# Performance work log

Measured on AMD Instinct MI355X. Metric: run time of the kernel, lower is better.

Reference implementation:

```python
import jax, jax.numpy as jnp
import numpy as np

N1, N2, E = 256, 128, 4096

def _conv(x, w, b):
    # NCHW conv, 3x3, padding=1 (SAME), then ReLU
    y = jax.lax.conv_general_dilated(x, w, (1, 1), 'SAME',
                                     dimension_numbers=('NCHW', 'OIHW', 'NCHW'))
    return jax.nn.relu(y + b[None, :, None, None])

def _pool(x):
    return jax.lax.reduce_window(x, -jnp.inf, jax.lax.max,
                                 (1, 1, 2, 2), (1, 1, 2, 2), 'VALID')

def _sage(x, src, dst, wl, bl, wr, n):
    # torch_geometric SAGEConv: out = lin_l(mean_j x_src) + lin_r(x), then L2 normalize
    agg = jax.ops.segment_sum(x[src], dst, num_segments=n)
    cnt = jax.ops.segment_sum(jnp.ones((src.shape[0],), x.dtype), dst, num_segments=n)
    agg = agg / jnp.maximum(cnt, 1.0)[:, None]
    out = agg @ wl.T + bl + x @ wr.T
    return out / jnp.maximum(jnp.linalg.norm(out, axis=-1, keepdims=True), 1e-12)

def _diff_pool(x, adj, s):
    # torch_geometric dense_diff_pool
    s = jax.nn.softmax(s, axis=-1)
    out = jnp.einsum('bnc,bnf->bcf', s, x)
    out_adj = jnp.einsum('bnc,bnm,bmd->bcd', s, adj, s)
    link = adj - jnp.einsum('bnc,bmc->bnm', s, s)
    link_loss = jnp.sqrt(jnp.sum(link * link)) / adj.size
    ent_loss = jnp.mean(jnp.sum(-s * jnp.log(s + 1e-15), axis=-1))
    return out, out_adj, link_loss, ent_loss

def setup_inputs() -> dict:
    key = jax.random.key(0)
    ks = jax.random.split(key, 16)
    rn = lambda k, shape, sc: jax.random.normal(k, shape, jnp.float32) * sc
    inp = {}
    inp['inputs'] = jax.random.normal(ks[0], (1, 5, 512, 512), jnp.float32)
    inp['edge_index'] = jax.random.randint(ks[1], (2, E), 0, N1)
    chans = [(5, 32), (32, 64), (64, 128), (128, 256), (256, 256)]
    for i, (ci, co) in enumerate(chans):
        inp[f'w{i+1}'] = rn(ks[2 + i], (co, ci, 3, 3), 1.0 / np.sqrt(ci * 9))
        inp[f'b{i+1}'] = jnp.zeros((co,), jnp.float32)
    sdims = [(256, 128), (256, 128), (128, 2)]
    for i, (ci, co) in enumerate(sdims):
        inp[f'sage{i+1}_wl'] = rn(ks[7 + 2 * i], (co, ci), 1.0 / np.sqrt(ci))
        inp[f'sage{i+1}_bl'] = jnp.zeros((co,), jnp.float32)
        inp[f'sage{i+1}_wr'] = rn(ks[8 + 2 * i], (co, ci), 1.0 / np.sqrt(ci))
    return inp

def reference(inputs, edge_index, w1, b1, w2, b2, w3, b3, w4, b4, w5, b5,
              sage1_wl, sage1_bl, sage1_wr, sage2_wl, sage2_bl, sage2_wr,
              sage3_wl, sage3_bl, sage3_wr):
    x = _pool(_conv(inputs, w1, b1))
    x = _pool(_conv(x, w2, b2))
    x = _pool(_conv(x, w3, b3))
    x = _pool(_conv(x, w4, b4))
    x = _pool(_conv(x, w5, b5))            # [1,256,16,16]
    org = x.reshape(N1, N1)                # [256 nodes, 256 feats]
    src, dst = edge_index[0], edge_index[1]
    x1 = _sage(org, src, dst, sage1_wl, sage1_bl, sage1_wr, N1)
    s1 = _sage(org, src, dst, sage2_wl, sage2_bl, sage2_wr, N1)
    # dense adjacency (scipy coo->dense sums duplicate edges)
    adj1 = jnp.zeros((N1, N1), jnp.float32).at[src, dst].add(1.0)
    xp, adjp, ll1, el1 = _diff_pool(x1[None], adj1[None], s1[None])
    xp = xp.reshape(N2, N2)
    adjp = adjp.reshape(N2, N2)
    # vectorized form of the per-row in-place argmax binarization loop
    row_max = jnp.max(adjp, axis=1, keepdims=True)
    edge_out = jnp.where(adjp == row_max, 1.0, 0.0)
    # dense_to_sparse of the binarized matrix (one max per row, generic case)
    cols = jnp.argmax(adjp, axis=1)
    ei2 = jnp.stack([jnp.arange(N2), cols])  # [2,128] int
    nodes_out = jnp.tanh(_sage(xp, ei2[0], ei2[1], sage3_wl, sage3_bl, sage3_wr, N2))
    adj2 = jnp.zeros((N2, N2), jnp.float32).at[ei2[0], ei2[1]].add(1.0)
    s2 = jnp.ones((1, N2, 1), jnp.float32)  # softmax over size-1 dim -> ones
    x2, _, ll2, el2 = _diff_pool(nodes_out[None], adj2[None], s2)
    return (x2.reshape(-1), ll1 + ll2, el1 + el2, nodes_out, edge_out, ei2)
```

## Files before the change

### kernel.cpp

```cpp
#include <hip/hip_runtime.h>
#include <hip/hip_bf16.h>
#include <math.h>

#define N_EDGES 4096
#define NN1 256
#define NN2 128

typedef short v8s __attribute__((ext_vector_type(8)));
typedef float v4f __attribute__((ext_vector_type(4)));

__device__ inline unsigned short f2b(float f){
  union { __hip_bfloat16 h; unsigned short u; } cv;
  cv.h = __float2bfloat16(f);
  return cv.u;
}

template<int NT>
__device__ inline float block_sum(float v, float* red, int t){
  red[t] = v; __syncthreads();
  #pragma unroll
  for (int st = NT/2; st > 0; st >>= 1){
    if (t < st) red[t] += red[t+st];
    __syncthreads();
  }
  float r = red[0]; __syncthreads();
  return r;
}
template<int NT>
__device__ inline float block_max(float v, float* red, int t){
  red[t] = v; __syncthreads();
  #pragma unroll
  for (int st = NT/2; st > 0; st >>= 1){
    if (t < st) red[t] = fmaxf(red[t], red[t+st]);
    __syncthreads();
  }
  float r = red[0]; __syncthreads();
  return r;
}
template<int NT>
__device__ inline int block_min_int(int v, int* red, int t){
  red[t] = v; __syncthreads();
  #pragma unroll
  for (int st = NT/2; st > 0; st >>= 1){
    if (t < st) red[t] = min(red[t], red[t+st]);
    __syncthreads();
  }
  int r = red[0]; __syncthreads();
  return r;
}

template<int CHUNKS, int COUT, int CIN, int SSLABS, int BSTR, int OUTF32>
__global__ __launch_bounds__(256) void conv_mfma(
    const unsigned short* __restrict__ in, const unsigned short* __restrict__ wb,
    const float* __restrict__ bias, unsigned short* __restrict__ outb,
    float* __restrict__ outf,
    int in_row, int in_slab, int out_row, int out_slab)
{
  constexpr int CG = COUT/32;
  __shared__ unsigned short tileb[SSLABS*2600];
  __shared__ unsigned short wldsb[9*32*40];

  const int cg = blockIdx.x % CG, bx = blockIdx.x / CG, by = blockIdx.y;
  const int tid = threadIdx.x, lane = tid & 63, wv = tid >> 6;
  const int cot = wv >> 1, wp = wv & 1;
  const int ml = lane & 15, g = lane >> 4;

  v4f acc[8];
  #pragma unroll
  for (int t = 0; t < 8; ++t) acc[t] = (v4f){0.f,0.f,0.f,0.f};

  for (int cb = 0; cb < CHUNKS; ++cb){
    if (cb) __syncthreads();
    for (int j = tid; j < SSLABS*324; j += 256){
      int s = j / 324, rem = j - s*324;
      int row = rem / 18, px = rem - row*18;
      int gidx = (cb*SSLABS + s)*in_slab + ((by*16 + row)*in_row + bx*16 + px)*8;
      *(v8s*)&tileb[s*2600 + (row*18+px)*8] = *(const v8s*)&in[gidx];
    }
    for (int j = tid; j < 1152; j += 256){
      int k = j >> 7, rem = j & 127;
      int co = rem >> 2, q = rem & 3;
      int gw = (k*COUT + cg*32 + co)*CIN + cb*32 + q*8;
      *(v8s*)&wldsb[(k*32+co)*40 + q*8] = *(const v8s*)&wb[gw];
    }
    __syncthreads();

    #pragma unroll
    for (int k9 = 0; k9 < 9; ++k9){
      const int ky = k9/3, kx = k9 - 3*(k9/3);
      v8s a = *(const v8s*)&wldsb[(k9*32 + cot*16 + ml)*40 + g*8];
      #pragma unroll
      for (int tt = 0; tt < 8; ++tt){
        int t = wp*8 + tt;
        v8s b = *(const v8s*)&tileb[g*BSTR + ((t+ky)*18 + kx + ml)*8];
        acc[tt] = __builtin_amdgcn_mfma_f32_16x16x32_bf16(a, b, acc[tt], 0, 0, 0);
      }
    }
  }

  const int cob = cg*32 + cot*16 + g*4;
  float b4[4] = {bias[cob], bias[cob+1], bias[cob+2], bias[cob+3]};
  #pragma unroll
  for (int tp = 0; tp < 4; ++tp){
    float m[4];
    #pragma unroll
    for (int r = 0; r < 4; ++r){
      float v = fmaxf(acc[2*tp][r], acc[2*tp+1][r]);
      float o = __shfl_xor(v, 1);
      m[r] = fmaxf(fmaxf(v, o) + b4[r], 0.f);
    }
    if ((lane & 1) == 0){
      int gy = by*8 + wp*4 + tp, gx = bx*8 + (ml >> 1);
      if (OUTF32){
        #pragma unroll
        for (int r = 0; r < 4; ++r)
          outf[(cob + r)*256 + gy*16 + gx] = m[r];
      } else {
        unsigned int u0 = (unsigned)f2b(m[0]) | ((unsigned)f2b(m[1]) << 16);
        unsigned int u1 = (unsigned)f2b(m[2]) | ((unsigned)f2b(m[3]) << 16);
        int slabo = cob >> 3, sub = (g & 1)*4;
        size_t idx = (size_t)slabo*out_slab + (size_t)((gy+1)*out_row + gx+1)*8 + sub;
        *(uint2*)(outb + idx) = make_uint2(u0, u1);
      }
    }
  }
}

__global__ __launch_bounds__(256) void zero_kernel(unsigned short* __restrict__ wsb,
                                                   float* __restrict__ adjz)
{
  int j = blockIdx.x*256 + threadIdx.x;
  const int c0=2056, c1=6184, c2=10344, c3=14568, c4=18920, ca=35368;
  if (j >= ca) return;
  if (j >= c4){
    int q = j - c4;
    ((float4*)adjz)[q] = make_float4(0.f,0.f,0.f,0.f);
    return;
  }
  int base, P, R, W, per, rem;
  if (j < c0)      { base=0;       P=516; R=514; W=512; per=2056; rem=j; }
  else if (j < c1) { base=2121792; P=260; R=258; W=256; per=1032; rem=j-c0; }
  else if (j < c2) { base=4268352; P=132; R=130; W=128; per=520;  rem=j-c1; }
  else if (j < c3) { base=5366592; P=68;  R=66;  W=64;  per=264;  rem=j-c2; }
  else             { base=5941056; P=36;  R=34;  W=32;  per=136;  rem=j-c3; }
  int s = rem / per, r2 = rem - s*per;
  int row, px;
  if (r2 < 2*P){ row = (r2 < P) ? 0 : R-1; px = (r2 < P) ? r2 : r2 - P; }
  else { int q = r2 - 2*P; row = 1 + (q >> 1); px = (q & 1) ? (W+1) : 0; }
  *(uint4*)&wsb[(size_t)base + ((size_t)(s*R + row)*P + px)*8] = make_uint4(0,0,0,0);
}

__global__ __launch_bounds__(256) void prep_kernel(
    const float* __restrict__ src, unsigned short* __restrict__ p0b,
    const float* __restrict__ w1, const float* __restrict__ w2,
    const float* __restrict__ w3, const float* __restrict__ w4,
    const float* __restrict__ w5, unsigned short* __restrict__ wbb,
    const float* __restrict__ a, const float* __restrict__ b2,
    const float* __restrict__ c2, const float* __restrict__ d2,
    float* __restrict__ o)
{
  int b = blockIdx.x, tid = threadIdx.x;
  if (b < 1024){
    int idx = b*256 + tid;
    int y = idx >> 9, x = idx & 511;
    unsigned short v8[8];
    #pragma unroll
    for (int c = 0; c < 5; ++c) v8[c] = f2b(src[c*262144 + y*512 + x]);
    v8[5] = 0; v8[6] = 0; v8[7] = 0;
    *(uint4*)&p0b[((size_t)(y+1)*516 + (x+1))*8] = *(uint4*)v8;
  } else if (b < 1452){
    int j = (b-1024)*256 + tid;
    int co, ci, CO, CIl, CIsrc, dst; const float* w;
    if (j < 1024)      { co=j>>5;        ci=j&31;        w=w1; CIsrc=5;   CO=32;  CIl=32;  dst=0; }
    else if (j < 3072) { int q=j-1024;   co=q>>5;  ci=q&31;  w=w2; CIsrc=32;  CO=64;  CIl=32;  dst=9216; }
    else if (j < 11264){ int q=j-3072;   co=q>>6;  ci=q&63;  w=w3; CIsrc=64;  CO=128; CIl=64;  dst=27648; }
    else if (j < 44032){ int q=j-11264;  co=q>>7;  ci=q&127; w=w4; CIsrc=128; CO=256; CIl=128; dst=101376; }
    else               { int q=j-44032;  co=q>>8;  ci=q&255; w=w5; CIsrc=256; CO=256; CIl=256; dst=396288; }
    #pragma unroll
    for (int k = 0; k < 9; ++k){
      float val = (ci < CIsrc) ? w[(co*CIsrc + ci)*9 + k] : 0.f;
      wbb[dst + (k*CO + co)*CIl + ci] = f2b(val);
    }
  } else {
    int idx = (b-1452)*256 + tid;
    int m = idx >> 15, rem = idx & 32767, k = rem >> 7, cc = rem & 127;
    const float* sp = (m==0)?a:(m==1)?b2:(m==2)?c2:d2;
    o[m*32768 + k*128 + cc] = sp[cc*256 + k];
  }
}

__global__ void build_adj_kernel(const int* __restrict__ ei, float* adj, float* cnt){
  int e = blockIdx.x*256 + threadIdx.x;
  if (e < N_EDGES){
    int s = ei[e], d = ei[N_EDGES + e];
    atomicAdd(&adj[s*NN1 + d], 1.0f);
    atomicAdd(&cnt[d], 1.0f);
  }
}

__global__ __launch_bounds__(128) void sage12_kernel(
    const float* __restrict__ adj, const float* __restrict__ cnt,
    const float* __restrict__ org,
    const float* __restrict__ wl1t, const float* __restrict__ bl1, const float* __restrict__ wr1t,
    const float* __restrict__ wl2t, const float* __restrict__ bl2, const float* __restrict__ wr2t,
    float* __restrict__ x1, float* __restrict__ s_out, float* __restrict__ st,
    float* __restrict__ entpart)
{
  __shared__ float sa[NN1], so[NN1], col[NN1], red[128];
  int n = blockIdx.x, c = threadIdx.x;
  for (int k = c; k < NN1; k += 128){
    col[k] = adj[k*NN1 + n];
    so[k]  = org[n*NN1 + k];
  }
  __syncthreads();
  float a0 = 0.f, a1 = 0.f;
  #pragma unroll 4
  for (int s2 = 0; s2 < NN1; ++s2){
    float av = col[s2];
    a0 += av * org[s2*NN1 + c];
    a1 += av * org[s2*NN1 + c + 128];
  }
  float cd = fmaxf(cnt[n], 1.0f);
  sa[c] = a0 / cd;
  sa[c+128] = a1 / cd;
  __syncthreads();

  float p1 = bl1[c], p2 = bl2[c];
  for (int k = 0; k < NN1; ++k){
    float av = sa[k], ov = so[k];
    p1 += av*wl1t[k*128+c] + ov*wr1t[k*128+c];
    p2 += av*wl2t[k*128+c] + ov*wr2t[k*128+c];
  }
  float n1s = block_sum<128>(p1*p1, red, c);
  x1[n*128 + c] = p1 / fmaxf(sqrtf(n1s), 1e-12f);
  float n2s = block_sum<128>(p2*p2, red, c);
  float p2n = p2 / fmaxf(sqrtf(n2s), 1e-12f);
  float mx = block_max<128>(p2n, red, c);
  float ev = expf(p2n - mx);
  float ssum = block_sum<128>(ev, red, c);
  float sv = ev / ssum;
  s_out[n*128 + c] = sv;
  st[c*NN1 + n] = sv;
  float esum = block_sum<128>(-sv * logf(sv + 1e-15f), red, c);
  if (c == 0) entpart[n] = esum;
}

__global__ __launch_bounds__(256) void fuse1_kernel(
    const float* __restrict__ s, const float* __restrict__ x1,
    const float* __restrict__ adj, const float* __restrict__ st,
    float* __restrict__ xp, float* __restrict__ t, float* __restrict__ linkpart)
{
  __shared__ float sn[128]; __shared__ float red[256];
  int b = blockIdx.x, tid = threadIdx.x;
  if (b < 64){
    int cc = b*2 + (tid >> 7), f = tid & 127;
    float acc = 0.f;
    for (int n = 0; n < NN1; ++n) acc += s[n*128+cc] * x1[n*128+f];
    xp[cc*128+f] = acc;
  } else if (b < 192){
    int n = (b-64)*2 + (tid >> 7), c = tid & 127;
    float acc = 0.f;
    for (int m = 0; m < NN1; ++m){
      float a = adj[n*NN1+m];
      if (a != 0.f) acc += a * s[m*128+c];
    }
    t[n*128+c] = acc;
  } else {
    int n = b - 192, m = tid;
    if (m < 128) sn[m] = s[n*128+m];
    __syncthreads();
    float dot = 0.f;
    for (int c = 0; c < 128; ++c) dot += sn[c]*st[c*NN1 + m];
    float v = adj[n*NN1+m] - dot;
    float part = block_sum<256>(v*v, red, m);
    if (m == 0) linkpart[n] = part;
  }
}

__global__ __launch_bounds__(128) void adjp_bin_kernel(
    const float* __restrict__ s, const float* __restrict__ t,
    float* __restrict__ edge_out, float* __restrict__ ei2_out, int* __restrict__ cols)
{
  __shared__ float scol[NN1]; __shared__ float red[128]; __shared__ int redi[128];
  int cc = blockIdx.x, j = threadIdx.x;
  scol[j]       = s[j*128 + cc];
  scol[j + 128] = s[(j+128)*128 + cc];
  __syncthreads();
  float acc = 0.f;
  for (int n = 0; n < NN1; ++n) acc += scol[n] * t[n*128 + j];
  float mx = block_max<128>(acc, red, j);
  edge_out[cc*128+j] = (acc == mx) ? 1.0f : 0.0f;
  int cand = (acc == mx) ? j : (1 << 30);
  int cmin = block_min_int<128>(cand, redi, j);
  if (j == 0){
    cols[cc] = cmin;
    ei2_out[cc] = (float)cc;
    ei2_out[128 + cc] = (float)cmin;
  }
}

__global__ __launch_bounds__(128) void sage3_kernel(
    const float* __restrict__ xp, const int* __restrict__ cols,
    const float* __restrict__ wl3, const float* __restrict__ bl3,
    const float* __restrict__ wr3, float* __restrict__ nodes_out)
{
  __shared__ int colsl[NN2]; __shared__ float red[128];
  int n = blockIdx.x, f = threadIdx.x;
  colsl[f] = cols[f];
  __syncthreads();
  float acc = 0.f, c = 0.f;
  for (int i = 0; i < NN2; ++i){
    if (colsl[i] == n){ acc += xp[i*128+f]; c += 1.f; }
  }
  float ag = acc / fmaxf(c, 1.f);
  float xv = xp[n*128+f];
  float q0 = block_sum<128>(ag*wl3[f]     + xv*wr3[f],     red, f);
  float q1 = block_sum<128>(ag*wl3[128+f] + xv*wr3[128+f], red, f);
  if (f == 0){
    float p0 = q0 + bl3[0], p1 = q1 + bl3[1];
    float nm = fmaxf(sqrtf(p0*p0 + p1*p1), 1e-12f);
    nodes_out[n*2+0] = tanhf(p0/nm);
    nodes_out[n*2+1] = tanhf(p1/nm);
  }
}

__global__ __launch_bounds__(256) void finalize_kernel(const float* __restrict__ linkpart,
    const float* __restrict__ entpart, float* __restrict__ d_out)
{
  __shared__ float red[256];
  int t = threadIdx.x;
  float ls = block_sum<256>(linkpart[t], red, t);
  float es = block_sum<256>(entpart[t], red, t);
  float v0 = 0.f, v1 = 0.f;
  if (t < 128){ v0 = d_out[4 + t*2 + 0]; v1 = d_out[4 + t*2 + 1]; }
  float s0 = block_sum<256>(v0, red, t);
  float s1 = block_sum<256>(v1, red, t);
  if (t == 0){
    d_out[0] = s0;
    d_out[1] = s1;
    d_out[2] = sqrtf(ls)/65536.0f + sqrtf(16256.0f)/16384.0f;
    d_out[3] = es/256.0f;
  }
}

extern "C" void kernel_launch(void* const* d_in, const int* in_sizes, int n_in,
                              void* d_out_v, int out_size, void* d_ws, size_t ws_size,
                              hipStream_t stream)
{
  (void)in_sizes; (void)n_in; (void)out_size; (void)ws_size;
  const float* input = (const float*)d_in[0];
  const int*   ei    = (const int*)  d_in[1];
  const float* w1 = (const float*)d_in[2];  const float* b1 = (const float*)d_in[3];
  const float* w2 = (const float*)d_in[4];  const float* b2 = (const float*)d_in[5];
  const float* w3 = (const float*)d_in[6];  const float* b3 = (const float*)d_in[7];
  const float* w4 = (const float*)d_in[8];  const float* b4 = (const float*)d_in[9];
  const float* w5 = (const float*)d_in[10]; const float* b5 = (const float*)d_in[11];
  const float* s1wl = (const float*)d_in[12]; const float* s1bl = (const float*)d_in[13];
  const float* s1wr = (const float*)d_in[14];
  const float* s2wl = (const float*)d_in[15]; const float* s2bl = (const float*)d_in[16];
  const float* s2wr = (const float*)d_in[17];
  const float* s3wl = (const float*)d_in[18]; const float* s3bl = (const float*)d_in[19];
  const float* s3wr = (const float*)d_in[20];
  float* d_out = (float*)d_out_v;
  float* ws = (float*)d_ws;

  unsigned short* P0b = (unsigned short*)(ws);
  unsigned short* Pb1 = (unsigned short*)(ws + 1060896);
  unsigned short* Pb2 = (unsigned short*)(ws + 2134176);
  unsigned short* Pb3 = (unsigned short*)(ws + 2683296);
  unsigned short* Pb4 = (unsigned short*)(ws + 2970528);
  unsigned short* wb  = (unsigned short*)(ws + 3127200);
  float* org = ws + 3620256;
  float* wt  = ws + 3685792;
  float* st  = ws + 3816864;
  float* G   = ws + 3849632;

  float* adj1     = G;
  float* cnt      = G + 65536;
  float* x1       = G + 147712;
  float* s        = G + 180480;
  float* t        = G + 213248;
  float* xp       = G + 246016;
  int*   cols     = (int*)(G + 278784);
  float* linkpart = G + 278912;
  float* entpart  = G + 279168;

  zero_kernel<<<dim3(139), 256, 0, stream>>>((unsigned short*)ws, adj1);
  prep_kernel<<<dim3(1964), 256, 0, stream>>>(input, P0b, w1, w2, w3, w4, w5, wb,
                                              s1wl, s1wr, s2wl, s2wr, wt);

  conv_mfma<1,32,32,1,0,0>      <<<dim3(32,32), 256, 0, stream>>>(P0b, wb,        b1, Pb1, nullptr, 516, 2121792, 260, 536640);
  conv_mfma<1,64,32,4,2600,0>   <<<dim3(32,16), 256, 0, stream>>>(Pb1, wb+9216,   b2, Pb2, nullptr, 260, 536640, 132, 137280);
  conv_mfma<2,128,64,4,2600,0>  <<<dim3(32,8),  256, 0, stream>>>(Pb2, wb+27648,  b3, Pb3, nullptr, 132, 137280, 68,  35904);
  conv_mfma<4,256,128,4,2600,0> <<<dim3(32,4),  256, 0, stream>>>(Pb3, wb+101376, b4, Pb4, nullptr, 68,  35904,  36,  9792);
  conv_mfma<8,256,256,4,2600,1> <<<dim3(16,2),  256, 0, stream>>>(Pb4, wb+396288, b5, nullptr, org, 36,  9792,   0,   0);

  build_adj_kernel<<<dim3(16),  256, 0, stream>>>(ei, adj1, cnt);
  sage12_kernel   <<<dim3(256), 128, 0, stream>>>(adj1, cnt, org, wt, s1bl, wt+32768,
                                                  wt+65536, s2bl, wt+98304, x1, s, st, entpart);
  fuse1_kernel    <<<dim3(448), 256, 0, stream>>>(s, x1, adj1, st, xp, t, linkpart);
  adjp_bin_kernel <<<dim3(128), 128, 0, stream>>>(s, t, d_out + 260, d_out + 16644, cols);
  sage3_kernel    <<<dim3(128), 128, 0, stream>>>(xp, cols, s3wl, s3bl, s3wr, d_out + 4);
  finalize_kernel <<<dim3(1),   256, 0, stream>>>(linkpart, entpart, d_out);
}
```

Measured before the change: 209.9 us.

## Double-buffer conv input tiles, load weights directly to registers, fold zeroing into prep

The conv kernel now double-buffers the input tile in shared memory, prefetching the next channel chunk into registers while the current chunk is computed, which removes one barrier per chunk. Weights are read straight from global memory into registers instead of being staged through a shared-memory tile. The separate zeroing kernel is merged into prep_kernel as extra blocks, saving one launch. In exchange, shared-memory use and register pressure go up, and the per-lane weight loads from global memory may be less coalesced.

```diff
diff --git a/kernel.cpp b/kernel.cpp
--- a/kernel.cpp
+++ b/kernel.cpp
@@ -56,45 +56,70 @@
     float* __restrict__ outf,
     int in_row, int in_slab, int out_row, int out_slab)
 {
-  constexpr int CG = COUT/32;
-  __shared__ unsigned short tileb[SSLABS*2600];
-  __shared__ unsigned short wldsb[9*32*40];
+  constexpr int CG  = COUT/32;
+  constexpr int TJ  = SSLABS*324;
+  constexpr int NST = (TJ + 255) / 256;
+  __shared__ unsigned short tileb[2][SSLABS*2600];
 
   const int cg = blockIdx.x % CG, bx = blockIdx.x / CG, by = blockIdx.y;
   const int tid = threadIdx.x, lane = tid & 63, wv = tid >> 6;
   const int cot = wv >> 1, wp = wv & 1;
   const int ml = lane & 15, g = lane >> 4;
 
-  v4f acc[8];
-  #pragma unroll
-  for (int t = 0; t < 8; ++t) acc[t] = (v4f){0.f,0.f,0.f,0.f};
-
-  for (int cb = 0; cb < CHUNKS; ++cb){
-    if (cb) __syncthreads();
-    for (int j = tid; j < SSLABS*324; j += 256){
+  int tsrc[NST], tlds[NST];
+  #pragma unroll
+  for (int s2 = 0; s2 < NST; ++s2){
+    int j = tid + s2*256;
+    if (j < TJ){
       int s = j / 324, rem = j - s*324;
       int row = rem / 18, px = rem - row*18;
-      int gidx = (cb*SSLABS + s)*in_slab + ((by*16 + row)*in_row + bx*16 + px)*8;
-      *(v8s*)&tileb[s*2600 + (row*18+px)*8] = *(const v8s*)&in[gidx];
-    }
-    for (int j = tid; j < 1152; j += 256){
-      int k = j >> 7, rem = j & 127;
-      int co = rem >> 2, q = rem & 3;
-      int gw = (k*COUT + cg*32 + co)*CIN + cb*32 + q*8;
-      *(v8s*)&wldsb[(k*32+co)*40 + q*8] = *(const v8s*)&wb[gw];
-    }
-    __syncthreads();
-
+      tsrc[s2] = s*in_slab + ((by*16 + row)*in_row + bx*16 + px)*8;
+      tlds[s2] = s*2600 + (row*18+px)*8;
+    } else { tsrc[s2] = -1; tlds[s2] = 0; }
+  }
+  const int wbase = (cg*32 + cot*16 + ml)*CIN + g*8;
+
+  v4f acc[8];
+  #pragma unroll
+  for (int t = 0; t < 8; ++t) acc[t] = (v4f){0.f,0.f,0.f,0.f};
+
+  uint4 rt[NST];
+  auto LD = [&](int cb){
+    int off = cb*SSLABS*in_slab;
+    #pragma unroll
+    for (int s2 = 0; s2 < NST; ++s2)
+      if (tsrc[s2] >= 0) rt[s2] = *(const uint4*)&in[tsrc[s2] + off];
+  };
+  auto ST = [&](int b){
+    #pragma unroll
+    for (int s2 = 0; s2 < NST; ++s2)
+      if (tsrc[s2] >= 0) *(uint4*)&tileb[b][tlds[s2]] = rt[s2];
+  };
+  auto COMPUTE = [&](int b, int cb){
+    v8s wa[9];
+    const int wo = wbase + cb*32;
+    #pragma unroll
+    for (int k = 0; k < 9; ++k)
+      wa[k] = *(const v8s*)&wb[k*COUT*CIN + wo];
     #pragma unroll
     for (int k9 = 0; k9 < 9; ++k9){
       const int ky = k9/3, kx = k9 - 3*(k9/3);
-      v8s a = *(const v8s*)&wldsb[(k9*32 + cot*16 + ml)*40 + g*8];
       #pragma unroll
       for (int tt = 0; tt < 8; ++tt){
         int t = wp*8 + tt;
-        v8s b = *(const v8s*)&tileb[g*BSTR + ((t+ky)*18 + kx + ml)*8];
-        acc[tt] = __builtin_amdgcn_mfma_f32_16x16x32_bf16(a, b, acc[tt], 0, 0, 0);
+        v8s bfr = *(const v8s*)&tileb[b][g*BSTR + ((t+ky)*18 + kx + ml)*8];
+        acc[tt] = __builtin_amdgcn_mfma_f32_16x16x32_bf16(wa[k9], bfr, acc[tt], 0, 0, 0);
       }
+    }
+  };
+
+  LD(0); ST(0); __syncthreads();
+  for (int cb = 0; cb < CHUNKS; ++cb){
+    if (cb + 1 < CHUNKS) LD(cb+1);
+    COMPUTE(cb & 1, cb);
+    if (cb + 1 < CHUNKS){
+      ST((cb+1) & 1);
+      __syncthreads();
     }
   }
 
@@ -126,30 +151,6 @@
   }
 }
 
-__global__ __launch_bounds__(256) void zero_kernel(unsigned short* __restrict__ wsb,
-                                                   float* __restrict__ adjz)
-{
-  int j = blockIdx.x*256 + threadIdx.x;
-  const int c0=2056, c1=6184, c2=10344, c3=14568, c4=18920, ca=35368;
-  if (j >= ca) return;
-  if (j >= c4){
-    int q = j - c4;
-    ((float4*)adjz)[q] = make_float4(0.f,0.f,0.f,0.f);
-    return;
-  }
-  int base, P, R, W, per, rem;
-  if (j < c0)      { base=0;       P=516; R=514; W=512; per=2056; rem=j; }
-  else if (j < c1) { base=2121792; P=260; R=258; W=256; per=1032; rem=j-c0; }
-  else if (j < c2) { base=4268352; P=132; R=130; W=128; per=520;  rem=j-c1; }
-  else if (j < c3) { base=5366592; P=68;  R=66;  W=64;  per=264;  rem=j-c2; }
-  else             { base=5941056; P=36;  R=34;  W=32;  per=136;  rem=j-c3; }
-  int s = rem / per, r2 = rem - s*per;
-  int row, px;
-  if (r2 < 2*P){ row = (r2 < P) ? 0 : R-1; px = (r2 < P) ? r2 : r2 - P; }
-  else { int q = r2 - 2*P; row = 1 + (q >> 1); px = (q & 1) ? (W+1) : 0; }
-  *(uint4*)&wsb[(size_t)base + ((size_t)(s*R + row)*P + px)*8] = make_uint4(0,0,0,0);
-}
-
 __global__ __launch_bounds__(256) void prep_kernel(
     const float* __restrict__ src, unsigned short* __restrict__ p0b,
     const float* __restrict__ w1, const float* __restrict__ w2,
@@ -157,7 +158,8 @@
     const float* __restrict__ w5, unsigned short* __restrict__ wbb,
     const float* __restrict__ a, const float* __restrict__ b2,
     const float* __restrict__ c2, const float* __restrict__ d2,
-    float* __restrict__ o)
+    float* __restrict__ o, unsigned short* __restrict__ wsb,
+    float* __restrict__ adjz)
 {
   int b = blockIdx.x, tid = threadIdx.x;
   if (b < 1024){
@@ -181,11 +183,31 @@
       float val = (ci < CIsrc) ? w[(co*CIsrc + ci)*9 + k] : 0.f;
       wbb[dst + (k*CO + co)*CIl + ci] = f2b(val);
     }
-  } else {
+  } else if (b < 1964){
     int idx = (b-1452)*256 + tid;
     int m = idx >> 15, rem = idx & 32767, k = rem >> 7, cc = rem & 127;
     const float* sp = (m==0)?a:(m==1)?b2:(m==2)?c2:d2;
     o[m*32768 + k*128 + cc] = sp[cc*256 + k];
+  } else {
+    int j = (b-1964)*256 + tid;
+    const int c0=2056, c1=6184, c2z=10344, c3=14568, c4=18920, ca=35368;
+    if (j >= ca) return;
+    if (j >= c4){
+      int q = j - c4;
+      ((float4*)adjz)[q] = make_float4(0.f,0.f,0.f,0.f);
+      return;
+    }
+    int base, P, R, W, per, rem;
+    if (j < c0)       { base=0;       P=516; R=514; W=512; per=2056; rem=j; }
+    else if (j < c1)  { base=2121792; P=260; R=258; W=256; per=1032; rem=j-c0; }
+    else if (j < c2z) { base=4268352; P=132; R=130; W=128; per=520;  rem=j-c1; }
+    else if (j < c3)  { base=5366592; P=68;  R=66;  W=64;  per=264;  rem=j-c2z; }
+    else              { base=5941056; P=36;  R=34;  W=32;  per=136;  rem=j-c3; }
+    int s = rem / per, r2 = rem - s*per;
+    int row, px;
+    if (r2 < 2*P){ row = (r2 < P) ? 0 : R-1; px = (r2 < P) ? r2 : r2 - P; }
+    else { int q = r2 - 2*P; row = 1 + (q >> 1); px = (q & 1) ? (W+1) : 0; }
+    *(uint4*)&wsb[(size_t)base + ((size_t)(s*R + row)*P + px)*8] = make_uint4(0,0,0,0);
   }
 }
 
@@ -385,9 +407,9 @@
   float* linkpart = G + 278912;
   float* entpart  = G + 279168;
 
-  zero_kernel<<<dim3(139), 256, 0, stream>>>((unsigned short*)ws, adj1);
-  prep_kernel<<<dim3(1964), 256, 0, stream>>>(input, P0b, w1, w2, w3, w4, w5, wb,
-                                              s1wl, s1wr, s2wl, s2wr, wt);
+  prep_kernel<<<dim3(2103), 256, 0, stream>>>(input, P0b, w1, w2, w3, w4, w5, wb,
+                                              s1wl, s1wr, s2wl, s2wr, wt,
+                                              (unsigned short*)ws, adj1);
 
   conv_mfma<1,32,32,1,0,0>      <<<dim3(32,32), 256, 0, stream>>>(P0b, wb,        b1, Pb1, nullptr, 516, 2121792, 260, 536640);
   conv_mfma<1,64,32,4,2600,0>   <<<dim3(32,16), 256, 0, stream>>>(Pb1, wb+9216,   b2, Pb2, nullptr, 260, 536640, 132, 137280);
```

Measured after the change: 219.8 us. 4.7% more time.

## Fuse graph tail kernels into one cooperative kernel and merge zeroing into prep

Applied to the files above, without the earlier changes.

Replaces the six small tail kernels (adjacency build, two SAGE layers, diff-pool fusion, argmax binarization, finalize) with one cooperative kernel of 256 blocks that uses grid-wide syncs between stages. It also folds the zero kernel into the prep kernel as extra blocks, so two fewer launches happen at the front. The aim is to remove launch and inter-kernel gap overhead in the latency-bound tail. In exchange there are five grid.sync barriers, and some stages leave half the threads idle because blocks are now 256 wide where the work was sized for 128.

```diff
diff --git a/kernel.cpp b/kernel.cpp
--- a/kernel.cpp
+++ b/kernel.cpp
@@ -1,6 +1,9 @@
 #include <hip/hip_runtime.h>
 #include <hip/hip_bf16.h>
+#include <hip/hip_cooperative_groups.h>
 #include <math.h>
+
+namespace cg = cooperative_groups;
 
 #define N_EDGES 4096
 #define NN1 256
@@ -15,33 +18,30 @@
   return cv.u;
 }
 
-template<int NT>
-__device__ inline float block_sum(float v, float* red, int t){
+__device__ inline float bsum(float v, float* red, int t){
   red[t] = v; __syncthreads();
   #pragma unroll
-  for (int st = NT/2; st > 0; st >>= 1){
+  for (int st = 128; st > 0; st >>= 1){
     if (t < st) red[t] += red[t+st];
     __syncthreads();
   }
   float r = red[0]; __syncthreads();
   return r;
 }
-template<int NT>
-__device__ inline float block_max(float v, float* red, int t){
+__device__ inline float bmax(float v, float* red, int t){
   red[t] = v; __syncthreads();
   #pragma unroll
-  for (int st = NT/2; st > 0; st >>= 1){
+  for (int st = 128; st > 0; st >>= 1){
     if (t < st) red[t] = fmaxf(red[t], red[t+st]);
     __syncthreads();
   }
   float r = red[0]; __syncthreads();
   return r;
 }
-template<int NT>
-__device__ inline int block_min_int(int v, int* red, int t){
+__device__ inline int bmin_i(int v, int* red, int t){
   red[t] = v; __syncthreads();
   #pragma unroll
-  for (int st = NT/2; st > 0; st >>= 1){
+  for (int st = 128; st > 0; st >>= 1){
     if (t < st) red[t] = min(red[t], red[t+st]);
     __syncthreads();
   }
@@ -126,30 +126,6 @@
   }
 }
 
-__global__ __launch_bounds__(256) void zero_kernel(unsigned short* __restrict__ wsb,
-                                                   float* __restrict__ adjz)
-{
-  int j = blockIdx.x*256 + threadIdx.x;
-  const int c0=2056, c1=6184, c2=10344, c3=14568, c4=18920, ca=35368;
-  if (j >= ca) return;
-  if (j >= c4){
-    int q = j - c4;
-    ((float4*)adjz)[q] = make_float4(0.f,0.f,0.f,0.f);
-    return;
-  }
-  int base, P, R, W, per, rem;
-  if (j < c0)      { base=0;       P=516; R=514; W=512; per=2056; rem=j; }
-  else if (j < c1) { base=2121792; P=260; R=258; W=256; per=1032; rem=j-c0; }
-  else if (j < c2) { base=4268352; P=132; R=130; W=128; per=520;  rem=j-c1; }
-  else if (j < c3) { base=5366592; P=68;  R=66;  W=64;  per=264;  rem=j-c2; }
-  else             { base=5941056; P=36;  R=34;  W=32;  per=136;  rem=j-c3; }
-  int s = rem / per, r2 = rem - s*per;
-  int row, px;
-  if (r2 < 2*P){ row = (r2 < P) ? 0 : R-1; px = (r2 < P) ? r2 : r2 - P; }
-  else { int q = r2 - 2*P; row = 1 + (q >> 1); px = (q & 1) ? (W+1) : 0; }
-  *(uint4*)&wsb[(size_t)base + ((size_t)(s*R + row)*P + px)*8] = make_uint4(0,0,0,0);
-}
-
 __global__ __launch_bounds__(256) void prep_kernel(
     const float* __restrict__ src, unsigned short* __restrict__ p0b,
     const float* __restrict__ w1, const float* __restrict__ w2,
@@ -157,7 +133,8 @@
     const float* __restrict__ w5, unsigned short* __restrict__ wbb,
     const float* __restrict__ a, const float* __restrict__ b2,
     const float* __restrict__ c2, const float* __restrict__ d2,
-    float* __restrict__ o)
+    float* __restrict__ o, unsigned short* __restrict__ wsb,
+    float* __restrict__ adjz)
 {
   int b = blockIdx.x, tid = threadIdx.x;
   if (b < 1024){
@@ -181,165 +158,183 @@
       float val = (ci < CIsrc) ? w[(co*CIsrc + ci)*9 + k] : 0.f;
       wbb[dst + (k*CO + co)*CIl + ci] = f2b(val);
     }
-  } else {
+  } else if (b < 1964){
     int idx = (b-1452)*256 + tid;
     int m = idx >> 15, rem = idx & 32767, k = rem >> 7, cc = rem & 127;
     const float* sp = (m==0)?a:(m==1)?b2:(m==2)?c2:d2;
     o[m*32768 + k*128 + cc] = sp[cc*256 + k];
-  }
-}
-
-__global__ void build_adj_kernel(const int* __restrict__ ei, float* adj, float* cnt){
-  int e = blockIdx.x*256 + threadIdx.x;
-  if (e < N_EDGES){
-    int s = ei[e], d = ei[N_EDGES + e];
-    atomicAdd(&adj[s*NN1 + d], 1.0f);
-    atomicAdd(&cnt[d], 1.0f);
-  }
-}
-
-__global__ __launch_bounds__(128) void sage12_kernel(
-    const float* __restrict__ adj, const float* __restrict__ cnt,
-    const float* __restrict__ org,
-    const float* __restrict__ wl1t, const float* __restrict__ bl1, const float* __restrict__ wr1t,
-    const float* __restrict__ wl2t, const float* __restrict__ bl2, const float* __restrict__ wr2t,
-    float* __restrict__ x1, float* __restrict__ s_out, float* __restrict__ st,
-    float* __restrict__ entpart)
+  } else {
+    int j = (b-1964)*256 + tid;
+    const int c0=2056, c1=6184, c2z=10344, c3=14568, c4=18920, ca=35368;
+    if (j >= ca) return;
+    if (j >= c4){
+      int q = j - c4;
+      ((float4*)adjz)[q] = make_float4(0.f,0.f,0.f,0.f);
+      return;
+    }
+    int base, P, R, W, per, rem;
+    if (j < c0)       { base=0;       P=516; R=514; W=512; per=2056; rem=j; }
+    else if (j < c1)  { base=2121792; P=260; R=258; W=256; per=1032; rem=j-c0; }
+    else if (j < c2z) { base=4268352; P=132; R=130; W=128; per=520;  rem=j-c1; }
+    else if (j < c3)  { base=5366592; P=68;  R=66;  W=64;  per=264;  rem=j-c2z; }
+    else              { base=5941056; P=36;  R=34;  W=32;  per=136;  rem=j-c3; }
+    int s = rem / per, r2 = rem - s*per;
+    int row, px;
+    if (r2 < 2*P){ row = (r2 < P) ? 0 : R-1; px = (r2 < P) ? r2 : r2 - P; }
+    else { int q = r2 - 2*P; row = 1 + (q >> 1); px = (q & 1) ? (W+1) : 0; }
+    *(uint4*)&wsb[(size_t)base + ((size_t)(s*R + row)*P + px)*8] = make_uint4(0,0,0,0);
+  }
+}
+
+__global__ __launch_bounds__(256) void coop_tail(
+    const int* ei, float* adj, float* cnt, const float* org, const float* wt,
+    const float* s1bl, const float* s2bl, float* x1, float* s, float* st,
+    float* entpart, float* xp, float* t, float* linkpart,
+    const float* s3wl, const float* s3bl, const float* s3wr,
+    float* d_out, int* cols)
 {
-  __shared__ float sa[NN1], so[NN1], col[NN1], red[128];
-  int n = blockIdx.x, c = threadIdx.x;
-  for (int k = c; k < NN1; k += 128){
-    col[k] = adj[k*NN1 + n];
-    so[k]  = org[n*NN1 + k];
-  }
-  __syncthreads();
-  float a0 = 0.f, a1 = 0.f;
-  #pragma unroll 4
-  for (int s2 = 0; s2 < NN1; ++s2){
-    float av = col[s2];
-    a0 += av * org[s2*NN1 + c];
-    a1 += av * org[s2*NN1 + c + 128];
-  }
-  float cd = fmaxf(cnt[n], 1.0f);
-  sa[c] = a0 / cd;
-  sa[c+128] = a1 / cd;
-  __syncthreads();
-
-  float p1 = bl1[c], p2 = bl2[c];
-  for (int k = 0; k < NN1; ++k){
-    float av = sa[k], ov = so[k];
-    p1 += av*wl1t[k*128+c] + ov*wr1t[k*128+c];
-    p2 += av*wl2t[k*128+c] + ov*wr2t[k*128+c];
-  }
-  float n1s = block_sum<128>(p1*p1, red, c);
-  x1[n*128 + c] = p1 / fmaxf(sqrtf(n1s), 1e-12f);
-  float n2s = block_sum<128>(p2*p2, red, c);
-  float p2n = p2 / fmaxf(sqrtf(n2s), 1e-12f);
-  float mx = block_max<128>(p2n, red, c);
-  float ev = expf(p2n - mx);
-  float ssum = block_sum<128>(ev, red, c);
-  float sv = ev / ssum;
-  s_out[n*128 + c] = sv;
-  st[c*NN1 + n] = sv;
-  float esum = block_sum<128>(-sv * logf(sv + 1e-15f), red, c);
-  if (c == 0) entpart[n] = esum;
-}
-
-__global__ __launch_bounds__(256) void fuse1_kernel(
-    const float* __restrict__ s, const float* __restrict__ x1,
-    const float* __restrict__ adj, const float* __restrict__ st,
-    float* __restrict__ xp, float* __restrict__ t, float* __restrict__ linkpart)
-{
-  __shared__ float sn[128]; __shared__ float red[256];
-  int b = blockIdx.x, tid = threadIdx.x;
-  if (b < 64){
-    int cc = b*2 + (tid >> 7), f = tid & 127;
+  cg::grid_group grid = cg::this_grid();
+  __shared__ float shA[256], shB[256], shC[256], shRed[256];
+  __shared__ int shRedI[256];
+  const int b = blockIdx.x, tid = threadIdx.x;
+
+  if (tid < 16){
+    int e = b*16 + tid;
+    int sn = ei[e], dn = ei[N_EDGES + e];
+    atomicAdd(&adj[sn*NN1 + dn], 1.0f);
+    atomicAdd(&cnt[dn], 1.0f);
+  }
+  grid.sync();
+
+  {
+    const int n = b;
+    const float* wl1t = wt;         const float* wr1t = wt + 32768;
+    const float* wl2t = wt + 65536; const float* wr2t = wt + 98304;
+    shC[tid] = adj[tid*NN1 + n];
+    shB[tid] = org[n*NN1 + tid];
+    __syncthreads();
+    float a0 = 0.f;
+    #pragma unroll 4
+    for (int s2 = 0; s2 < NN1; ++s2) a0 += shC[s2] * org[s2*NN1 + tid];
+    float cd = fmaxf(cnt[n], 1.0f);
+    shA[tid] = a0 / cd;
+    __syncthreads();
+
+    const int c = tid & 127;
+    float p1 = 0.f, p2 = 0.f;
+    if (tid < 128){
+      p1 = s1bl[c]; p2 = s2bl[c];
+      for (int k = 0; k < NN1; ++k){
+        float av = shA[k], ov = shB[k];
+        p1 += av*wl1t[k*128+c] + ov*wr1t[k*128+c];
+        p2 += av*wl2t[k*128+c] + ov*wr2t[k*128+c];
+      }
+    }
+    float n1s = bsum(tid < 128 ? p1*p1 : 0.f, shRed, tid);
+    if (tid < 128) x1[n*128 + c] = p1 / fmaxf(sqrtf(n1s), 1e-12f);
+    float n2s = bsum(tid < 128 ? p2*p2 : 0.f, shRed, tid);
+    float p2n = p2 / fmaxf(sqrtf(n2s), 1e-12f);
+    float mx = bmax(tid < 128 ? p2n : -INFINITY, shRed, tid);
+    float ev = expf(p2n - mx);
+    float ssum = bsum(tid < 128 ? ev : 0.f, shRed, tid);
+    float sv = ev / ssum;
+    if (tid < 128){
+      s[n*128 + c] = sv;
+      st[c*NN1 + n] = sv;
+    }
+    float esum = bsum(tid < 128 ? (-sv * logf(sv + 1e-15f)) : 0.f, shRed, tid);
+    if (tid == 0) entpart[n] = esum;
+  }
+  grid.sync();
+
+  {
+    if (b < 64){
+      int cc = b*2 + (tid >> 7), f = tid & 127;
+      float acc = 0.f;
+      for (int n2 = 0; n2 < NN1; ++n2) acc += s[n2*128+cc] * x1[n2*128+f];
+      xp[cc*128+f] = acc;
+    } else if (b < 192){
+      int n2 = (b-64)*2 + (tid >> 7), c = tid & 127;
+      float acc = 0.f;
+      for (int m = 0; m < NN1; ++m){
+        float a = adj[n2*NN1+m];
+        if (a != 0.f) acc += a * s[m*128+c];
+      }
+      t[n2*128+c] = acc;
+    }
+    __syncthreads();
+    if (tid < 128) shC[tid] = s[b*128 + tid];
+    __syncthreads();
+    float dot = 0.f;
+    for (int c2 = 0; c2 < 128; ++c2) dot += shC[c2]*st[c2*NN1 + tid];
+    float v = adj[b*NN1+tid] - dot;
+    float part = bsum(v*v, shRed, tid);
+    if (tid == 0) linkpart[b] = part;
+  }
+  grid.sync();
+
+  if (b < 128){
+    int cc = b;
+    shA[tid] = s[tid*128 + cc];
+    __syncthreads();
     float acc = 0.f;
-    for (int n = 0; n < NN1; ++n) acc += s[n*128+cc] * x1[n*128+f];
-    xp[cc*128+f] = acc;
-  } else if (b < 192){
-    int n = (b-64)*2 + (tid >> 7), c = tid & 127;
-    float acc = 0.f;
-    for (int m = 0; m < NN1; ++m){
-      float a = adj[n*NN1+m];
-      if (a != 0.f) acc += a * s[m*128+c];
-    }
-    t[n*128+c] = acc;
-  } else {
-    int n = b - 192, m = tid;
-    if (m < 128) sn[m] = s[n*128+m];
-    __syncthreads();
-    float dot = 0.f;
-    for (int c = 0; c < 128; ++c) dot += sn[c]*st[c*NN1 + m];
-    float v = adj[n*NN1+m] - dot;
-    float part = block_sum<256>(v*v, red, m);
-    if (m == 0) linkpart[n] = part;
-  }
-}
-
-__global__ __launch_bounds__(128) void adjp_bin_kernel(
-    const float* __restrict__ s, const float* __restrict__ t,
-    float* __restrict__ edge_out, float* __restrict__ ei2_out, int* __restrict__ cols)
-{
-  __shared__ float scol[NN1]; __shared__ float red[128]; __shared__ int redi[128];
-  int cc = blockIdx.x, j = threadIdx.x;
-  scol[j]       = s[j*128 + cc];
-  scol[j + 128] = s[(j+128)*128 + cc];
-  __syncthreads();
-  float acc = 0.f;
-  for (int n = 0; n < NN1; ++n) acc += scol[n] * t[n*128 + j];
-  float mx = block_max<128>(acc, red, j);
-  edge_out[cc*128+j] = (acc == mx) ? 1.0f : 0.0f;
-  int cand = (acc == mx) ? j : (1 << 30);
-  int cmin = block_min_int<128>(cand, redi, j);
-  if (j == 0){
-    cols[cc] = cmin;
-    ei2_out[cc] = (float)cc;
-    ei2_out[128 + cc] = (float)cmin;
-  }
-}
-
-__global__ __launch_bounds__(128) void sage3_kernel(
-    const float* __restrict__ xp, const int* __restrict__ cols,
-    const float* __restrict__ wl3, const float* __restrict__ bl3,
-    const float* __restrict__ wr3, float* __restrict__ nodes_out)
-{
-  __shared__ int colsl[NN2]; __shared__ float red[128];
-  int n = blockIdx.x, f = threadIdx.x;
-  colsl[f] = cols[f];
-  __syncthreads();
-  float acc = 0.f, c = 0.f;
-  for (int i = 0; i < NN2; ++i){
-    if (colsl[i] == n){ acc += xp[i*128+f]; c += 1.f; }
-  }
-  float ag = acc / fmaxf(c, 1.f);
-  float xv = xp[n*128+f];
-  float q0 = block_sum<128>(ag*wl3[f]     + xv*wr3[f],     red, f);
-  float q1 = block_sum<128>(ag*wl3[128+f] + xv*wr3[128+f], red, f);
-  if (f == 0){
-    float p0 = q0 + bl3[0], p1 = q1 + bl3[1];
-    float nm = fmaxf(sqrtf(p0*p0 + p1*p1), 1e-12f);
-    nodes_out[n*2+0] = tanhf(p0/nm);
-    nodes_out[n*2+1] = tanhf(p1/nm);
-  }
-}
-
-__global__ __launch_bounds__(256) void finalize_kernel(const float* __restrict__ linkpart,
-    const float* __restrict__ entpart, float* __restrict__ d_out)
-{
-  __shared__ float red[256];
-  int t = threadIdx.x;
-  float ls = block_sum<256>(linkpart[t], red, t);
-  float es = block_sum<256>(entpart[t], red, t);
-  float v0 = 0.f, v1 = 0.f;
-  if (t < 128){ v0 = d_out[4 + t*2 + 0]; v1 = d_out[4 + t*2 + 1]; }
-  float s0 = block_sum<256>(v0, red, t);
-  float s1 = block_sum<256>(v1, red, t);
-  if (t == 0){
-    d_out[0] = s0;
-    d_out[1] = s1;
-    d_out[2] = sqrtf(ls)/65536.0f + sqrtf(16256.0f)/16384.0f;
-    d_out[3] = es/256.0f;
+    int j = tid & 127;
+    if (tid < 128){
+      for (int n2 = 0; n2 < NN1; ++n2) acc += shA[n2] * t[n2*128 + j];
+    }
+    float mx = bmax(tid < 128 ? acc : -INFINITY, shRed, tid);
+    if (tid < 128) d_out[260 + cc*128 + j] = (acc == mx) ? 1.0f : 0.0f;
+    int cand = (tid < 128 && acc == mx) ? j : (1 << 30);
+    int cmin = bmin_i(cand, shRedI, tid);
+    if (tid == 0){
+      cols[cc] = cmin;
+      d_out[16644 + cc]       = (float)cc;
+      d_out[16644 + 128 + cc] = (float)cmin;
+    }
+  }
+  grid.sync();
+
+  if (b < 128){
+    int n = b;
+    if (tid < 128) shRedI[tid] = cols[tid];
+    __syncthreads();
+    float q0in = 0.f, q1in = 0.f;
+    if (tid < 128){
+      int f = tid;
+      float acc = 0.f, c = 0.f;
+      for (int i = 0; i < NN2; ++i){
+        if (shRedI[i] == n){ acc += xp[i*128+f]; c += 1.f; }
+      }
+      float ag = acc / fmaxf(c, 1.f);
+      float xv = xp[n*128+f];
+      q0in = ag*s3wl[f]     + xv*s3wr[f];
+      q1in = ag*s3wl[128+f] + xv*s3wr[128+f];
+    }
+    __syncthreads();
+    float q0 = bsum(q0in, shRed, tid);
+    float q1 = bsum(q1in, shRed, tid);
+    if (tid == 0){
+      float p0 = q0 + s3bl[0], p1 = q1 + s3bl[1];
+      float nm = fmaxf(sqrtf(p0*p0 + p1*p1), 1e-12f);
+      d_out[4 + n*2+0] = tanhf(p0/nm);
+      d_out[4 + n*2+1] = tanhf(p1/nm);
+    }
+  }
+  grid.sync();
+
+  if (b == 0){
+    float ls = bsum(linkpart[tid], shRed, tid);
+    float es = bsum(entpart[tid], shRed, tid);
+    float v0 = 0.f, v1 = 0.f;
+    if (tid < 128){ v0 = d_out[4 + tid*2 + 0]; v1 = d_out[4 + tid*2 + 1]; }
+    float s0 = bsum(v0, shRed, tid);
+    float s1 = bsum(v1, shRed, tid);
+    if (tid == 0){
+      d_out[0] = s0;
+      d_out[1] = s1;
+      d_out[2] = sqrtf(ls)/65536.0f + sqrtf(16256.0f)/16384.0f;
+      d_out[3] = es/256.0f;
+    }
   }
 }
 
@@ -385,9 +380,9 @@
   float* linkpart = G + 278912;
   float* entpart  = G + 279168;
 
-  zero_kernel<<<dim3(139), 256, 0, stream>>>((unsigned short*)ws, adj1);
-  prep_kernel<<<dim3(1964), 256, 0, stream>>>(input, P0b, w1, w2, w3, w4, w5, wb,
-                                              s1wl, s1wr, s2wl, s2wr, wt);
+  prep_kernel<<<dim3(2103), 256, 0, stream>>>(input, P0b, w1, w2, w3, w4, w5, wb,
+                                              s1wl, s1wr, s2wl, s2wr, wt,
+                                              (unsigned short*)ws, adj1);
 
   conv_mfma<1,32,32,1,0,0>      <<<dim3(32,32), 256, 0, stream>>>(P0b, wb,        b1, Pb1, nullptr, 516, 2121792, 260, 536640);
   conv_mfma<1,64,32,4,2600,0>   <<<dim3(32,16), 256, 0, stream>>>(Pb1, wb+9216,   b2, Pb2, nullptr, 260, 536640, 132, 137280);
@@ -395,11 +390,9 @@
   conv_mfma<4,256,128,4,2600,0> <<<dim3(32,4),  256, 0, stream>>>(Pb3, wb+101376, b4, Pb4, nullptr, 68,  35904,  36,  9792);
   conv_mfma<8,256,256,4,2600,1> <<<dim3(16,2),  256, 0, stream>>>(Pb4, wb+396288, b5, nullptr, org, 36,  9792,   0,   0);
 
-  build_adj_kernel<<<dim3(16),  256, 0, stream>>>(ei, adj1, cnt);
-  sage12_kernel   <<<dim3(256), 128, 0, stream>>>(adj1, cnt, org, wt, s1bl, wt+32768,
-                                                  wt+65536, s2bl, wt+98304, x1, s, st, entpart);
-  fuse1_kernel    <<<dim3(448), 256, 0, stream>>>(s, x1, adj1, st, xp, t, linkpart);
-  adjp_bin_kernel <<<dim3(128), 128, 0, stream>>>(s, t, d_out + 260, d_out + 16644, cols);
-  sage3_kernel    <<<dim3(128), 128, 0, stream>>>(xp, cols, s3wl, s3bl, s3wr, d_out + 4);
-  finalize_kernel <<<dim3(1),   256, 0, stream>>>(linkpart, entpart, d_out);
-}
+  void* args[] = { (void*)&ei, (void*)&adj1, (void*)&cnt, (void*)&org, (void*)&wt,
+                   (void*)&s1bl, (void*)&s2bl, (void*)&x1, (void*)&s, (void*)&st,
+                   (void*)&entpart, (void*)&xp, (void*)&t, (void*)&linkpart,
+                   (void*)&s3wl, (void*)&s3bl, (void*)&s3wr, (void*)&d_out, (void*)&cols };
+  hipLaunchCooperativeKernel((void*)coop_tail, dim3(256), dim3(256), args, 0, stream);
+}
```

Result: slower. 336.4 us (+60.3%).

## Split-K the two deepest convs and fold zeroing into prep kernel

Applied to the files above, without the earlier changes.

The conv4 and conv5 layers now split the input-channel reduction across blockIdx.z (2 and 8 ways). Each split writes unpooled fp32 partial sums to a workspace, and a new reduce_pool kernel sums the partials and applies bias, ReLU and 2x2 max-pool. This raises the block count for layers that previously launched only 128 and 32 blocks, to make better use of the GPU's compute units. It costs extra global traffic for the partials and two extra launches. Separately, the padding and adjacency zeroing is merged into prep_kernel as extra blocks, which removes one launch.

```diff
diff --git a/kernel.cpp b/kernel.cpp
--- a/kernel.cpp
+++ b/kernel.cpp
@@ -49,7 +49,7 @@
   return r;
 }
 
-template<int CHUNKS, int COUT, int CIN, int SSLABS, int BSTR, int OUTF32>
+template<int CHUNKS, int COUT, int CIN, int SSLABS, int BSTR, int OUTMODE>
 __global__ __launch_bounds__(256) void conv_mfma(
     const unsigned short* __restrict__ in, const unsigned short* __restrict__ wb,
     const float* __restrict__ bias, unsigned short* __restrict__ outb,
@@ -61,6 +61,8 @@
   __shared__ unsigned short wldsb[9*32*40];
 
   const int cg = blockIdx.x % CG, bx = blockIdx.x / CG, by = blockIdx.y;
+  const int z = blockIdx.z;
+  const int cbase = z*CHUNKS;
   const int tid = threadIdx.x, lane = tid & 63, wv = tid >> 6;
   const int cot = wv >> 1, wp = wv & 1;
   const int ml = lane & 15, g = lane >> 4;
@@ -74,13 +76,13 @@
     for (int j = tid; j < SSLABS*324; j += 256){
       int s = j / 324, rem = j - s*324;
       int row = rem / 18, px = rem - row*18;
-      int gidx = (cb*SSLABS + s)*in_slab + ((by*16 + row)*in_row + bx*16 + px)*8;
+      int gidx = ((cbase+cb)*SSLABS + s)*in_slab + ((by*16 + row)*in_row + bx*16 + px)*8;
       *(v8s*)&tileb[s*2600 + (row*18+px)*8] = *(const v8s*)&in[gidx];
     }
     for (int j = tid; j < 1152; j += 256){
       int k = j >> 7, rem = j & 127;
       int co = rem >> 2, q = rem & 3;
-      int gw = (k*COUT + cg*32 + co)*CIN + cb*32 + q*8;
+      int gw = (k*COUT + cg*32 + co)*CIN + (cbase+cb)*32 + q*8;
       *(v8s*)&wldsb[(k*32+co)*40 + q*8] = *(const v8s*)&wb[gw];
     }
     __syncthreads();
@@ -99,6 +101,18 @@
   }
 
   const int cob = cg*32 + cot*16 + g*4;
+  if (OUTMODE == 2){
+    const int W = out_row;
+    #pragma unroll
+    for (int tt = 0; tt < 8; ++tt){
+      int gy = by*16 + wp*8 + tt, gx = bx*16 + ml;
+      #pragma unroll
+      for (int r = 0; r < 4; ++r)
+        outf[((size_t)(z*COUT + cob + r)*W + gy)*W + gx] = acc[tt][r];
+    }
+    return;
+  }
+
   float b4[4] = {bias[cob], bias[cob+1], bias[cob+2], bias[cob+3]};
   #pragma unroll
   for (int tp = 0; tp < 4; ++tp){
@@ -111,7 +125,7 @@
     }
     if ((lane & 1) == 0){
       int gy = by*8 + wp*4 + tp, gx = bx*8 + (ml >> 1);
-      if (OUTF32){
+      if (OUTMODE == 1){
         #pragma unroll
         for (int r = 0; r < 4; ++r)
           outf[(cob + r)*256 + gy*16 + gx] = m[r];
@@ -126,28 +140,30 @@
   }
 }
 
-__global__ __launch_bounds__(256) void zero_kernel(unsigned short* __restrict__ wsb,
-                                                   float* __restrict__ adjz)
-{
-  int j = blockIdx.x*256 + threadIdx.x;
-  const int c0=2056, c1=6184, c2=10344, c3=14568, c4=18920, ca=35368;
-  if (j >= ca) return;
-  if (j >= c4){
-    int q = j - c4;
-    ((float4*)adjz)[q] = make_float4(0.f,0.f,0.f,0.f);
-    return;
-  }
-  int base, P, R, W, per, rem;
-  if (j < c0)      { base=0;       P=516; R=514; W=512; per=2056; rem=j; }
-  else if (j < c1) { base=2121792; P=260; R=258; W=256; per=1032; rem=j-c0; }
-  else if (j < c2) { base=4268352; P=132; R=130; W=128; per=520;  rem=j-c1; }
-  else if (j < c3) { base=5366592; P=68;  R=66;  W=64;  per=264;  rem=j-c2; }
-  else             { base=5941056; P=36;  R=34;  W=32;  per=136;  rem=j-c3; }
-  int s = rem / per, r2 = rem - s*per;
-  int row, px;
-  if (r2 < 2*P){ row = (r2 < P) ? 0 : R-1; px = (r2 < P) ? r2 : r2 - P; }
-  else { int q = r2 - 2*P; row = 1 + (q >> 1); px = (q & 1) ? (W+1) : 0; }
-  *(uint4*)&wsb[(size_t)base + ((size_t)(s*R + row)*P + px)*8] = make_uint4(0,0,0,0);
+template<int SPLITK, int OUTF32>
+__global__ __launch_bounds__(256) void reduce_pool(
+    const float* __restrict__ pbuf, const float* __restrict__ bias,
+    unsigned short* __restrict__ outb, float* __restrict__ outf,
+    int COUT, int H, int W, int out_row, int out_slab)
+{
+  int idx = blockIdx.x*256 + threadIdx.x;
+  const int OW = W >> 1, OH = H >> 1;
+  if (idx >= COUT*OH*OW) return;
+  int px = idx % OW; int t2 = idx / OW; int py = t2 % OH; int cout = t2 / OH;
+  size_t base = ((size_t)cout*H + 2*py)*W + 2*px;
+  size_t sstr = (size_t)COUT*H*W;
+  float s00=0.f, s01=0.f, s10=0.f, s11=0.f;
+  #pragma unroll
+  for (int s = 0; s < SPLITK; ++s){
+    const float* pb = pbuf + s*sstr + base;
+    s00 += pb[0]; s01 += pb[1]; s10 += pb[W]; s11 += pb[W+1];
+  }
+  float m = fmaxf(fmaxf(fmaxf(s00,s01), fmaxf(s10,s11)) + bias[cout], 0.f);
+  if (OUTF32){
+    outf[cout*OH*OW + py*OW + px] = m;
+  } else {
+    outb[(size_t)(cout>>3)*out_slab + (size_t)((py+1)*out_row + px+1)*8 + (cout&7)] = f2b(m);
+  }
 }
 
 __global__ __launch_bounds__(256) void prep_kernel(
@@ -157,7 +173,8 @@
     const float* __restrict__ w5, unsigned short* __restrict__ wbb,
     const float* __restrict__ a, const float* __restrict__ b2,
     const float* __restrict__ c2, const float* __restrict__ d2,
-    float* __restrict__ o)
+    float* __restrict__ o, unsigned short* __restrict__ wsb,
+    float* __restrict__ adjz)
 {
   int b = blockIdx.x, tid = threadIdx.x;
   if (b < 1024){
@@ -181,11 +198,31 @@
       float val = (ci < CIsrc) ? w[(co*CIsrc + ci)*9 + k] : 0.f;
       wbb[dst + (k*CO + co)*CIl + ci] = f2b(val);
     }
-  } else {
+  } else if (b < 1964){
     int idx = (b-1452)*256 + tid;
     int m = idx >> 15, rem = idx & 32767, k = rem >> 7, cc = rem & 127;
     const float* sp = (m==0)?a:(m==1)?b2:(m==2)?c2:d2;
     o[m*32768 + k*128 + cc] = sp[cc*256 + k];
+  } else {
+    int j = (b-1964)*256 + tid;
+    const int c0=2056, c1=6184, c2z=10344, c3=14568, c4=18920, ca=35368;
+    if (j >= ca) return;
+    if (j >= c4){
+      int q = j - c4;
+      ((float4*)adjz)[q] = make_float4(0.f,0.f,0.f,0.f);
+      return;
+    }
+    int base, P, R, W, per, rem;
+    if (j < c0)       { base=0;       P=516; R=514; W=512; per=2056; rem=j; }
+    else if (j < c1)  { base=2121792; P=260; R=258; W=256; per=1032; rem=j-c0; }
+    else if (j < c2z) { base=4268352; P=132; R=130; W=128; per=520;  rem=j-c1; }
+    else if (j < c3)  { base=5366592; P=68;  R=66;  W=64;  per=264;  rem=j-c2z; }
+    else              { base=5941056; P=36;  R=34;  W=32;  per=136;  rem=j-c3; }
+    int s = rem / per, r2 = rem - s*per;
+    int row, px;
+    if (r2 < 2*P){ row = (r2 < P) ? 0 : R-1; px = (r2 < P) ? r2 : r2 - P; }
+    else { int q = r2 - 2*P; row = 1 + (q >> 1); px = (q & 1) ? (W+1) : 0; }
+    *(uint4*)&wsb[(size_t)base + ((size_t)(s*R + row)*P + px)*8] = make_uint4(0,0,0,0);
   }
 }
 
@@ -384,16 +421,19 @@
   int*   cols     = (int*)(G + 278784);
   float* linkpart = G + 278912;
   float* entpart  = G + 279168;
-
-  zero_kernel<<<dim3(139), 256, 0, stream>>>((unsigned short*)ws, adj1);
-  prep_kernel<<<dim3(1964), 256, 0, stream>>>(input, P0b, w1, w2, w3, w4, w5, wb,
-                                              s1wl, s1wr, s2wl, s2wr, wt);
-
-  conv_mfma<1,32,32,1,0,0>      <<<dim3(32,32), 256, 0, stream>>>(P0b, wb,        b1, Pb1, nullptr, 516, 2121792, 260, 536640);
-  conv_mfma<1,64,32,4,2600,0>   <<<dim3(32,16), 256, 0, stream>>>(Pb1, wb+9216,   b2, Pb2, nullptr, 260, 536640, 132, 137280);
-  conv_mfma<2,128,64,4,2600,0>  <<<dim3(32,8),  256, 0, stream>>>(Pb2, wb+27648,  b3, Pb3, nullptr, 132, 137280, 68,  35904);
-  conv_mfma<4,256,128,4,2600,0> <<<dim3(32,4),  256, 0, stream>>>(Pb3, wb+101376, b4, Pb4, nullptr, 68,  35904,  36,  9792);
-  conv_mfma<8,256,256,4,2600,1> <<<dim3(16,2),  256, 0, stream>>>(Pb4, wb+396288, b5, nullptr, org, 36,  9792,   0,   0);
+  float* PART     = ws + 4129280;
+
+  prep_kernel<<<dim3(2103), 256, 0, stream>>>(input, P0b, w1, w2, w3, w4, w5, wb,
+                                              s1wl, s1wr, s2wl, s2wr, wt,
+                                              (unsigned short*)ws, adj1);
+
+  conv_mfma<1,32,32,1,0,0>      <<<dim3(32,32),   256, 0, stream>>>(P0b, wb,        b1, Pb1, nullptr, 516, 2121792, 260, 536640);
+  conv_mfma<1,64,32,4,2600,0>   <<<dim3(32,16),   256, 0, stream>>>(Pb1, wb+9216,   b2, Pb2, nullptr, 260, 536640, 132, 137280);
+  conv_mfma<2,128,64,4,2600,0>  <<<dim3(32,8),    256, 0, stream>>>(Pb2, wb+27648,  b3, Pb3, nullptr, 132, 137280, 68,  35904);
+  conv_mfma<2,256,128,4,2600,2> <<<dim3(32,4,2),  256, 0, stream>>>(Pb3, wb+101376, b4, nullptr, PART, 68, 35904, 64, 0);
+  reduce_pool<2,0>              <<<dim3(1024),    256, 0, stream>>>(PART, b4, Pb4, nullptr, 256, 64, 64, 36, 9792);
+  conv_mfma<1,256,256,4,2600,2> <<<dim3(16,2,8),  256, 0, stream>>>(Pb4, wb+396288, b5, nullptr, PART, 36, 9792, 32, 0);
+  reduce_pool<8,1>              <<<dim3(256),     256, 0, stream>>>(PART, b5, nullptr, org, 256, 32, 32, 0, 0);
 
   build_adj_kernel<<<dim3(16),  256, 0, stream>>>(ei, adj1, cnt);
   sage12_kernel   <<<dim3(256), 128, 0, stream>>>(adj1, cnt, org, wt, s1bl, wt+32768,
```

Measured after the change: 178.7 us (median of 3 runs). -14.9%, faster.
